# Optimization experiments

Hardware: AMD Instinct MI355X
Metric: run time of the kernel (lower is better)

## Reference

```python
import jax, jax.numpy as jnp
import numpy as np

DIM = 256; HEADS = 8; DEPTH = 2; DFF = 128
T = 64      # timesteps (transformer batch dim for s_transformer)
N = 2048    # total agents
S = 256     # number of segments (scenes)
L = 8       # agents per segment (N = S*L)
HD = DIM // HEADS
LN_EPS = 1e-5


def _ln(x, w, b):
    m = x.mean(-1, keepdims=True)
    v = x.var(-1, keepdims=True)
    return (x - m) / jnp.sqrt(v + LN_EPS) * w + b


def _mha(x, qkvw, qkvb, ow, ob):
    B, Sq, D = x.shape
    qkv = x @ qkvw.T + qkvb                      # [B,Sq,3D]
    q, k, v = jnp.split(qkv, 3, axis=-1)
    def sp(t):
        return t.reshape(B, Sq, HEADS, HD).transpose(0, 2, 1, 3)
    q, k, v = sp(q), sp(k), sp(v)
    a = jax.nn.softmax(jnp.einsum('bhqd,bhkd->bhqk', q, k) * (1.0 / (HD ** 0.5)))
    o = jnp.einsum('bhqk,bhkd->bhqd', a, v).transpose(0, 2, 1, 3).reshape(B, Sq, D)
    return o @ ow.T + ob


def _layer(x, qkvw, qkvb, ow, ob, l1w, l1b, l2w, l2b, ln1w, ln1b, ln2w, ln2b):
    # PyTorch TransformerEncoderLayer, post-norm, relu FFN
    x = _ln(x + _mha(x, qkvw, qkvb, ow, ob), ln1w, ln1b)
    h = jax.nn.relu(x @ l1w.T + l1b) @ l2w.T + l2b
    return _ln(x + h, ln2w, ln2b)


def _encoder(x, qkvw, qkvb, ow, ob, l1w, l1b, l2w, l2b, ln1w, ln1b, ln2w, ln2b):
    for i in range(DEPTH):
        x = _layer(x, qkvw[i], qkvb[i], ow[i], ob[i], l1w[i], l1b[i],
                   l2w[i], l2b[i], ln1w[i], ln1b[i], ln2w[i], ln2b[i])
    return x


def setup_inputs() -> dict:
    key = jax.random.key(0)
    ks = iter(jax.random.split(key, 64))
    def rn(shape, scale=0.05):
        return jax.random.normal(next(ks), shape, dtype=jnp.float32) * scale
    inp = {}
    inp['moveinfo'] = jax.random.normal(next(ks), (N, T, 2), dtype=jnp.float32)
    starts = jnp.arange(S, dtype=jnp.int32) * L
    inp['seq_start_end'] = jnp.stack([starts, starts + L], axis=1)  # [S,2]
    inp['w_in'] = rn((DIM, 2)); inp['b_in'] = rn((DIM,))
    for p in ('s', 't'):
        inp[p + '_qkvw'] = rn((DEPTH, 3 * DIM, DIM)); inp[p + '_qkvb'] = rn((DEPTH, 3 * DIM))
        inp[p + '_ow'] = rn((DEPTH, DIM, DIM)); inp[p + '_ob'] = rn((DEPTH, DIM))
        inp[p + '_l1w'] = rn((DEPTH, DFF, DIM)); inp[p + '_l1b'] = rn((DEPTH, DFF))
        inp[p + '_l2w'] = rn((DEPTH, DIM, DFF)); inp[p + '_l2b'] = rn((DEPTH, DIM))
        inp[p + '_ln1w'] = jnp.ones((DEPTH, DIM)); inp[p + '_ln1b'] = jnp.zeros((DEPTH, DIM))
        inp[p + '_ln2w'] = jnp.ones((DEPTH, DIM)); inp[p + '_ln2b'] = jnp.zeros((DEPTH, DIM))
    return inp


def reference(moveinfo, seq_start_end, w_in, b_in,
              s_qkvw, s_qkvb, s_ow, s_ob, s_l1w, s_l1b, s_l2w, s_l2b,
              s_ln1w, s_ln1b, s_ln2w, s_ln2b,
              t_qkvw, t_qkvb, t_ow, t_ob, t_l1w, t_l1b, t_l2w, t_l2b,
              t_ln1w, t_ln1b, t_ln2w, t_ln2b):
    # to_dim: Linear(2, dim) + exact GELU
    s_in = jax.nn.gelu(jnp.einsum('ntc,dc->ntd', moveinfo, w_in) + b_in, approximate=False)
    s_in = s_in.transpose(1, 0, 2)                       # [T, N, D]
    # gather equal-length segments: ragged loop batched as one attention call
    idx = seq_start_end[:, 0][:, None] + jnp.arange(L)   # [S, L]
    seg = s_in[:, idx, :].reshape(T * S, L, DIM)         # [T*S, L, D]
    cls = jnp.full((T * S, 1, DIM), 1e-5, dtype=s_in.dtype)
    x = jnp.concatenate([cls, seg], axis=1)              # [T*S, 1+L, D]
    x = _encoder(x, s_qkvw, s_qkvb, s_ow, s_ob, s_l1w, s_l1b, s_l2w, s_l2b,
                 s_ln1w, s_ln1b, s_ln2w, s_ln2b)
    t_in = x[:, 0, :].reshape(T, S, DIM).transpose(1, 0, 2)  # [S, T, D]
    out = _encoder(t_in, t_qkvw, t_qkvb, t_ow, t_ob, t_l1w, t_l1b, t_l2w, t_l2b,
                   t_ln1w, t_ln1b, t_ln2w, t_ln2b)
    return out
```

## Files before the change

### kernel.cpp

```cpp
#include <hip/hip_runtime.h>
#include <hip/hip_bf16.h>
#include <math.h>

typedef __bf16 bf16_t;
typedef float floatx4 __attribute__((ext_vector_type(4)));
typedef bf16_t bf16x8 __attribute__((ext_vector_type(8)));

typedef __attribute__((address_space(1))) void g_void;
typedef __attribute__((address_space(3))) void lds_void;

__device__ __forceinline__ void ldg_lds16(const bf16_t* g, bf16_t* l) {
    __builtin_amdgcn_global_load_lds((g_void*)g, (lds_void*)l, 16, 0, 0);
}

__device__ __forceinline__ void unpack4(uint2 r, float* o) {
    o[0] = __uint_as_float((r.x & 0xffffu) << 16); o[1] = __uint_as_float(r.x & 0xffff0000u);
    o[2] = __uint_as_float((r.y & 0xffffu) << 16); o[3] = __uint_as_float(r.y & 0xffff0000u);
}

__global__ void cvt_weights(const float* __restrict__ sqkvw, const float* __restrict__ sow,
                            const float* __restrict__ sl1w,  const float* __restrict__ sl2w,
                            const float* __restrict__ tqkvw, const float* __restrict__ tow,
                            const float* __restrict__ tl1w,  const float* __restrict__ tl2w,
                            bf16_t* __restrict__ dst) {
    int i = blockIdx.x * 256 + threadIdx.x;
    float v;
    if      (i <  393216) v = sqkvw[i];
    else if (i <  524288) v = sow  [i -  393216];
    else if (i <  589824) v = sl1w [i -  524288];
    else if (i <  655360) v = sl2w [i -  589824];
    else if (i < 1048576) v = tqkvw[i -  655360];
    else if (i < 1179648) v = tow  [i - 1048576];
    else if (i < 1245184) v = tl1w [i - 1179648];
    else                  v = tl2w [i - 1245184];
    dst[i] = (bf16_t)v;
}

__global__ void embed_k(const float* __restrict__ mv, const float* __restrict__ w_in,
                        const float* __restrict__ b_in, bf16_t* __restrict__ x, int b0) {
    int blk = blockIdx.x; int d = threadIdx.x;
    int tok = blk % 9; int lb = blk / 9;
    size_t oidx = (size_t)blk * 256 + d;
    if (tok == 0) { x[oidx] = (bf16_t)1e-5f; return; }
    int bb = b0 + lb; int t = bb >> 8; int s = bb & 255;
    int n = s * 8 + (tok - 1);
    float m0 = mv[((size_t)n * 64 + t) * 2];
    float m1 = mv[((size_t)n * 64 + t) * 2 + 1];
    float v = m0 * w_in[2 * d] + m1 * w_in[2 * d + 1] + b_in[d];
    v = 0.5f * v * (1.0f + erff(v * 0.70710678118654752f));
    x[oidx] = (bf16_t)v;
}

__global__ __launch_bounds__(256) void gemm_bt(const bf16_t* __restrict__ A,
                                               const bf16_t* __restrict__ W,
                                               const float* __restrict__ bias,
                                               bf16_t* __restrict__ C,
                                               int M, int N, int K, int relu) {
    __shared__ __align__(16) bf16_t As[8192];
    __shared__ __align__(16) bf16_t Ws[8192];
    int MT = M >> 7, NT = N >> 7;
    int g = blockIdx.x;
    int m_t, n_t;
    if ((MT & 7) == 0) {
        int x = g & 7, q = g >> 3;
        m_t = (q / NT) * 8 + x;
        n_t = q % NT;
    } else {
        m_t = g / NT; n_t = g % NT;
    }
    int tid = threadIdx.x;
    int lane = tid & 63;
    int wave = tid >> 6;
    int m0 = m_t * 128;
    int n0 = n_t * 128;
    int wm = (wave & 1) * 64;
    int wn = (wave >> 1) * 64;
    int arow = tid >> 2;
    int acol = (tid & 3) * 8;
    int fm = lane & 15;
    int fq = lane >> 4;

    floatx4 acc[4][4] = {};

    const bf16_t* Ag = A + (size_t)(m0 + arow) * K + acol;
    const bf16_t* Wg = W + (size_t)(n0 + arow) * K + acol;

    for (int k0 = 0; k0 < K; k0 += 64) {
        __syncthreads();
        ldg_lds16(Ag + k0,                       &As[tid * 8]);
        ldg_lds16(Ag + k0 + (size_t)64 * K,      &As[2048 + tid * 8]);
        ldg_lds16(Ag + k0 + 32,                  &As[4096 + tid * 8]);
        ldg_lds16(Ag + k0 + 32 + (size_t)64 * K, &As[6144 + tid * 8]);
        ldg_lds16(Wg + k0,                       &Ws[tid * 8]);
        ldg_lds16(Wg + k0 + (size_t)64 * K,      &Ws[2048 + tid * 8]);
        ldg_lds16(Wg + k0 + 32,                  &Ws[4096 + tid * 8]);
        ldg_lds16(Wg + k0 + 32 + (size_t)64 * K, &Ws[6144 + tid * 8]);
        __syncthreads();

#pragma unroll
        for (int sl = 0; sl < 2; sl++) {
            int base = sl * 4096;
            bf16x8 af[4], wf[4];
#pragma unroll
            for (int mi = 0; mi < 4; mi++)
                af[mi] = *(const bf16x8*)&As[base + (wm + mi * 16 + fm) * 32 + fq * 8];
#pragma unroll
            for (int ni = 0; ni < 4; ni++)
                wf[ni] = *(const bf16x8*)&Ws[base + (wn + ni * 16 + fm) * 32 + fq * 8];
#pragma unroll
            for (int mi = 0; mi < 4; mi++)
#pragma unroll
                for (int ni = 0; ni < 4; ni++)
                    acc[mi][ni] = __builtin_amdgcn_mfma_f32_16x16x32_bf16(wf[ni], af[mi], acc[mi][ni], 0, 0, 0);
        }
    }

#pragma unroll
    for (int mi = 0; mi < 4; mi++) {
        int row = m0 + wm + mi * 16 + fm;
#pragma unroll
        for (int ni = 0; ni < 4; ni++) {
            int colb = n0 + wn + ni * 16 + fq * 4;
            float4 b4 = *(const float4*)(bias + colb);
            float v0 = acc[mi][ni][0] + b4.x;
            float v1 = acc[mi][ni][1] + b4.y;
            float v2 = acc[mi][ni][2] + b4.z;
            float v3 = acc[mi][ni][3] + b4.w;
            if (relu) {
                v0 = fmaxf(v0, 0.f); v1 = fmaxf(v1, 0.f);
                v2 = fmaxf(v2, 0.f); v3 = fmaxf(v3, 0.f);
            }
            bf16_t t4[4] = {(bf16_t)v0, (bf16_t)v1, (bf16_t)v2, (bf16_t)v3};
            *(uint2*)(C + (size_t)row * N + colb) = *(uint2*)t4;
        }
    }
}

__device__ __forceinline__ void epi_resln64(
    floatx4 (&acc)[4][4], int m0, int wn, int fm, int fq, int wave,
    const float* __restrict__ bias, const bf16_t* __restrict__ res_bf,
    const float* __restrict__ res_f, const float* __restrict__ lnw,
    const float* __restrict__ lnb, bf16_t* out_bf, float* out_f,
    bf16_t* cls_bf, float* cls_f, int b0,
    float (*rs)[64], float (*rss)[64]) {
    float s[4] = {0.f, 0.f, 0.f, 0.f}, ss[4] = {0.f, 0.f, 0.f, 0.f};
#pragma unroll
    for (int mi = 0; mi < 4; mi++) {
        size_t row = (size_t)(m0 + mi * 16 + fm);
#pragma unroll
        for (int ni = 0; ni < 4; ni++) {
            int col = wn + ni * 16 + fq * 4;
            float4 b4 = *(const float4*)(bias + col);
            float r4[4];
            if (res_f) {
                float4 t = *(const float4*)(res_f + row * 256 + col);
                r4[0] = t.x; r4[1] = t.y; r4[2] = t.z; r4[3] = t.w;
            } else {
                unpack4(*(const uint2*)(res_bf + row * 256 + col), r4);
            }
            float v0 = acc[mi][ni][0] + b4.x + r4[0];
            float v1 = acc[mi][ni][1] + b4.y + r4[1];
            float v2 = acc[mi][ni][2] + b4.z + r4[2];
            float v3 = acc[mi][ni][3] + b4.w + r4[3];
            acc[mi][ni][0] = v0; acc[mi][ni][1] = v1;
            acc[mi][ni][2] = v2; acc[mi][ni][3] = v3;
            s[mi] += v0 + v1 + v2 + v3;
            ss[mi] += v0 * v0 + v1 * v1 + v2 * v2 + v3 * v3;
        }
    }
#pragma unroll
    for (int mi = 0; mi < 4; mi++) {
        s[mi]  += __shfl_xor(s[mi], 16);  s[mi]  += __shfl_xor(s[mi], 32);
        ss[mi] += __shfl_xor(ss[mi], 16); ss[mi] += __shfl_xor(ss[mi], 32);
    }
    if (fq == 0) {
#pragma unroll
        for (int mi = 0; mi < 4; mi++) {
            rs [wave][mi * 16 + fm] = s[mi];
            rss[wave][mi * 16 + fm] = ss[mi];
        }
    }
    __syncthreads();
#pragma unroll
    for (int mi = 0; mi < 4; mi++) {
        int lrow = mi * 16 + fm;
        int grow = m0 + lrow;
        size_t row = (size_t)grow;
        float mean = (rs[0][lrow] + rs[1][lrow] + rs[2][lrow] + rs[3][lrow]) * (1.f / 256.f);
        float var  = (rss[0][lrow] + rss[1][lrow] + rss[2][lrow] + rss[3][lrow]) * (1.f / 256.f)
                   - mean * mean;
        float inv = rsqrtf(var + 1e-5f);
        int is_cls = (cls_bf != nullptr) && (grow % 9 == 0);
        size_t di = 0;
        if (is_cls) {
            int bb = b0 + grow / 9;
            int tt = bb >> 8, sseg = bb & 255;
            di = ((size_t)(sseg * 64 + tt)) * 256;
        }
#pragma unroll
        for (int ni = 0; ni < 4; ni++) {
            int col = wn + ni * 16 + fq * 4;
            float4 w4 = *(const float4*)(lnw + col);
            float4 bl = *(const float4*)(lnb + col);
            float o0 = (acc[mi][ni][0] - mean) * inv * w4.x + bl.x;
            float o1 = (acc[mi][ni][1] - mean) * inv * w4.y + bl.y;
            float o2 = (acc[mi][ni][2] - mean) * inv * w4.z + bl.z;
            float o3 = (acc[mi][ni][3] - mean) * inv * w4.w + bl.w;
            if (out_bf) {
                bf16_t t4[4] = {(bf16_t)o0, (bf16_t)o1, (bf16_t)o2, (bf16_t)o3};
                *(uint2*)(out_bf + row * 256 + col) = *(uint2*)t4;
            }
            if (out_f) {
                float4 t; t.x = o0; t.y = o1; t.z = o2; t.w = o3;
                *(float4*)(out_f + row * 256 + col) = t;
            }
            if (is_cls) {
                bf16_t t4[4] = {(bf16_t)o0, (bf16_t)o1, (bf16_t)o2, (bf16_t)o3};
                *(uint2*)(cls_bf + di + col) = *(uint2*)t4;
                float4 t; t.x = o0; t.y = o1; t.z = o2; t.w = o3;
                *(float4*)(cls_f + di + col) = t;
            }
        }
    }
}

__global__ __launch_bounds__(256) void gemm_proj_ln(const bf16_t* __restrict__ A,
                                                    const bf16_t* __restrict__ W,
                                                    const float* __restrict__ bias,
                                                    const bf16_t* __restrict__ res_bf,
                                                    const float* __restrict__ res_f,
                                                    const float* __restrict__ lnw,
                                                    const float* __restrict__ lnb,
                                                    bf16_t* out_bf,
                                                    float* out_f) {
    __shared__ __align__(16) bf16_t As[4096];
    __shared__ __align__(16) bf16_t Ws[16384];
    __shared__ float rs[4][64], rss[4][64];
    int tid = threadIdx.x;
    int lane = tid & 63, wave = tid >> 6;
    int m0 = blockIdx.x * 64;
    int wn = wave * 64;
    int fm = lane & 15, fq = lane >> 4;
    floatx4 acc[4][4] = {};
    const bf16_t* Ag = A + (size_t)(m0 + (tid >> 2)) * 256 + (tid & 3) * 8;
    const bf16_t* Wg = W + (size_t)(tid >> 2) * 256 + (tid & 3) * 8;

    auto STAGE = [&](int r, int b) {
        int k = r * 32;
        ldg_lds16(Ag + k, &As[b * 2048 + tid * 8]);
#pragma unroll
        for (int j = 0; j < 4; j++)
            ldg_lds16(Wg + k + j * 16384, &Ws[b * 8192 + j * 2048 + tid * 8]);
    };
    auto COMPUTE = [&](int b) {
        bf16x8 af[4], wf[4];
#pragma unroll
        for (int mi = 0; mi < 4; mi++)
            af[mi] = *(const bf16x8*)&As[b * 2048 + (mi * 16 + fm) * 32 + fq * 8];
#pragma unroll
        for (int ni = 0; ni < 4; ni++)
            wf[ni] = *(const bf16x8*)&Ws[b * 8192 + (wn + ni * 16 + fm) * 32 + fq * 8];
#pragma unroll
        for (int mi = 0; mi < 4; mi++)
#pragma unroll
            for (int ni = 0; ni < 4; ni++)
                acc[mi][ni] = __builtin_amdgcn_mfma_f32_16x16x32_bf16(wf[ni], af[mi], acc[mi][ni], 0, 0, 0);
    };

    STAGE(0, 0);
    __syncthreads();
    for (int r = 0; r < 7; ++r) {
        STAGE(r + 1, (r + 1) & 1);
        COMPUTE(r & 1);
        __syncthreads();
    }
    COMPUTE(1);
    epi_resln64(acc, m0, wn, fm, fq, wave, bias, res_bf, res_f, lnw, lnb,
                out_bf, out_f, nullptr, nullptr, 0, rs, rss);
}

__global__ __launch_bounds__(256) void gemm_ffn_ln(const bf16_t* __restrict__ X,
                                                   const bf16_t* __restrict__ w1,
                                                   const float* __restrict__ b1,
                                                   const bf16_t* __restrict__ w2,
                                                   const float* __restrict__ b2,
                                                   const float* __restrict__ lnw,
                                                   const float* __restrict__ lnb,
                                                   const float* __restrict__ res_f,
                                                   bf16_t* out_bf, float* out_f,
                                                   bf16_t* cls_bf, float* cls_f, int b0) {
    __shared__ __align__(16) bf16_t As[4096];
    __shared__ __align__(16) bf16_t Ws[8192];
    __shared__ __align__(16) bf16_t Hs[10240];
    __shared__ float rs[4][64], rss[4][64];
    int tid = threadIdx.x, lane = tid & 63, wave = tid >> 6;
    int m0 = blockIdx.x * 64;
    int wn1 = wave * 32;
    int wn2 = wave * 64;
    int fm = lane & 15, fq = lane >> 4;
    floatx4 acc[4][2] = {};
    const bf16_t* Ag = X + (size_t)(m0 + (tid >> 2)) * 256 + (tid & 3) * 8;
    const bf16_t* Wg = w1 + (size_t)(tid >> 2) * 256 + (tid & 3) * 8;

    auto STAGE = [&](int r, int b) {
        int k = r * 32;
        ldg_lds16(Ag + k, &As[b * 2048 + tid * 8]);
#pragma unroll
        for (int j = 0; j < 2; j++)
            ldg_lds16(Wg + k + j * 16384, &Ws[b * 4096 + j * 2048 + tid * 8]);
    };
    auto COMPUTE = [&](int b) {
        bf16x8 af[4], wf[2];
#pragma unroll
        for (int mi = 0; mi < 4; mi++)
            af[mi] = *(const bf16x8*)&As[b * 2048 + (mi * 16 + fm) * 32 + fq * 8];
#pragma unroll
        for (int ni = 0; ni < 2; ni++)
            wf[ni] = *(const bf16x8*)&Ws[b * 4096 + (wn1 + ni * 16 + fm) * 32 + fq * 8];
#pragma unroll
        for (int mi = 0; mi < 4; mi++)
#pragma unroll
            for (int ni = 0; ni < 2; ni++)
                acc[mi][ni] = __builtin_amdgcn_mfma_f32_16x16x32_bf16(wf[ni], af[mi], acc[mi][ni], 0, 0, 0);
    };

    STAGE(0, 0);
    __syncthreads();
    for (int r = 0; r < 7; ++r) {
        STAGE(r + 1, (r + 1) & 1);
        COMPUTE(r & 1);
        __syncthreads();
    }
    COMPUTE(1);

#pragma unroll
    for (int mi = 0; mi < 4; mi++) {
        int row = mi * 16 + fm;
#pragma unroll
        for (int ni = 0; ni < 2; ni++) {
            int c = wn1 + ni * 16 + fq * 4;
            float4 b4 = *(const float4*)(b1 + c);
            bf16_t t4[4];
            t4[0] = (bf16_t)fmaxf(acc[mi][ni][0] + b4.x, 0.f);
            t4[1] = (bf16_t)fmaxf(acc[mi][ni][1] + b4.y, 0.f);
            t4[2] = (bf16_t)fmaxf(acc[mi][ni][2] + b4.z, 0.f);
            t4[3] = (bf16_t)fmaxf(acc[mi][ni][3] + b4.w, 0.f);
            *(uint2*)&Hs[(c >> 5) * 2560 + row * 40 + (c & 31)] = *(uint2*)t4;
        }
    }
    __syncthreads();
    floatx4 acc2[4][4] = {};
#pragma unroll
    for (int ks = 0; ks < 4; ks++) {
        bf16x8 af2[4];
#pragma unroll
        for (int mi = 0; mi < 4; mi++)
            af2[mi] = *(const bf16x8*)&Hs[ks * 2560 + (mi * 16 + fm) * 40 + fq * 8];
#pragma unroll
        for (int ni = 0; ni < 4; ni++) {
            bf16x8 wf2 = *(const bf16x8*)(w2 + (size_t)(wn2 + ni * 16 + fm) * 128 + ks * 32 + fq * 8);
#pragma unroll
            for (int mi = 0; mi < 4; mi++)
                acc2[mi][ni] = __builtin_amdgcn_mfma_f32_16x16x32_bf16(wf2, af2[mi], acc2[mi][ni], 0, 0, 0);
        }
    }
    epi_resln64(acc2, m0, wn2, fm, fq, wave, b2, X, res_f, lnw, lnb,
                out_bf, out_f, cls_bf, cls_f, b0, rs, rss);
}

__global__ __launch_bounds__(320) void attn9_k(const bf16_t* __restrict__ qkv,
                                               bf16_t* __restrict__ ao) {
    __shared__ __align__(16) bf16_t kv[36 * 512];
    int b = blockIdx.x; int tid = threadIdx.x;
    const bf16_t* src = qkv + (size_t)b * 27648;
    for (int c = tid; c < 2304; c += 320) {
        int row = c >> 6; int off = (c & 63) << 3;
        *(uint4*)&kv[row * 512 + off] = *(const uint4*)&src[row * 768 + 256 + off];
    }
    __syncthreads();
    if (tid < 288) {
        int s = tid / 72; int rem = tid - s * 72; int h = rem / 9; int i = rem - h * 9;
        const bf16_t* qp = src + (size_t)(s * 9 + i) * 768 + h * 32;
        float qf[32];
#pragma unroll
        for (int c = 0; c < 4; c++) {
            bf16x8 t8 = *(const bf16x8*)(qp + c * 8);
#pragma unroll
            for (int e = 0; e < 8; e++) qf[c * 8 + e] = (float)t8[e];
        }
        float sc[9]; float mx = -1e30f;
#pragma unroll
        for (int j = 0; j < 9; j++) {
            const bf16_t* kp = &kv[(s * 9 + j) * 512 + h * 32];
            float d = 0.f;
#pragma unroll
            for (int c = 0; c < 4; c++) {
                bf16x8 t8 = *(const bf16x8*)(kp + c * 8);
#pragma unroll
                for (int e = 0; e < 8; e++) d += qf[c * 8 + e] * (float)t8[e];
            }
            d *= 0.17677669529663687f;
            sc[j] = d; mx = fmaxf(mx, d);
        }
        float den = 0.f;
#pragma unroll
        for (int j = 0; j < 9; j++) { sc[j] = __expf(sc[j] - mx); den += sc[j]; }
        float inv = 1.0f / den;
        float of[32] = {};
#pragma unroll
        for (int j = 0; j < 9; j++) {
            const bf16_t* vp = &kv[(s * 9 + j) * 512 + 256 + h * 32];
            float w = sc[j];
#pragma unroll
            for (int c = 0; c < 4; c++) {
                bf16x8 t8 = *(const bf16x8*)(vp + c * 8);
#pragma unroll
                for (int e = 0; e < 8; e++) of[c * 8 + e] += w * (float)t8[e];
            }
        }
        bf16_t* dst = ao + ((size_t)(b * 4 + s) * 9 + i) * 256 + h * 32;
#pragma unroll
        for (int c = 0; c < 4; c++) {
            bf16x8 o8;
#pragma unroll
            for (int e = 0; e < 8; e++) o8[e] = (bf16_t)(of[c * 8 + e] * inv);
            *(bf16x8*)(dst + c * 8) = o8;
        }
    }
}

__global__ __launch_bounds__(256) void attn64_k(const bf16_t* __restrict__ qkv,
                                                bf16_t* __restrict__ ao) {
    __shared__ __align__(16) float kk[64 * 36];
    __shared__ __align__(16) float vv[64 * 36];
    __shared__ __align__(16) float pp[64 * 64];
    __shared__ float mloc[4 * 64];
    __shared__ float sloc[4 * 64];
    int s = blockIdx.x >> 3, h = blockIdx.x & 7;
    int t = threadIdx.x;
    int i = t & 63;
    int wq = t >> 6;

    {
        int r = t >> 2, c = t & 3;
        const bf16_t* kb = qkv + ((size_t)(s * 64 + r)) * 768 + h * 32 + 256 + c * 8;
        bf16x8 k8 = *(const bf16x8*)kb;
        bf16x8 v8 = *(const bf16x8*)(kb + 256);
        float* kd = &kk[r * 36 + c * 8];
        float* vd = &vv[r * 36 + c * 8];
#pragma unroll
        for (int e = 0; e < 8; e++) { kd[e] = (float)k8[e]; vd[e] = (float)v8[e]; }
    }
    const bf16_t* qb = qkv + ((size_t)(s * 64 + i)) * 768 + h * 32;
    float qf[32];
#pragma unroll
    for (int c = 0; c < 4; c++) {
        bf16x8 t8 = *(const bf16x8*)(qb + c * 8);
#pragma unroll
        for (int e = 0; e < 8; e++) qf[c * 8 + e] = (float)t8[e];
    }
    __syncthreads();

    float sc[16]; float mx = -1e30f;
#pragma unroll
    for (int jj = 0; jj < 16; jj++) {
        int j = wq * 16 + jj;
        const float* kr = &kk[j * 36];
        float d = 0.f;
#pragma unroll
        for (int c = 0; c < 8; c++) {
            float4 k4 = *(const float4*)(kr + c * 4);
            d += qf[c*4+0]*k4.x + qf[c*4+1]*k4.y + qf[c*4+2]*k4.z + qf[c*4+3]*k4.w;
        }
        d *= 0.17677669529663687f;
        sc[jj] = d; mx = fmaxf(mx, d);
    }
    float se = 0.f;
#pragma unroll
    for (int jj = 0; jj < 16; jj++) se += __expf(sc[jj] - mx);
    mloc[wq * 64 + i] = mx;
    sloc[wq * 64 + i] = se;
    __syncthreads();

    float m0 = mloc[i], m1 = mloc[64 + i], m2 = mloc[128 + i], m3 = mloc[192 + i];
    float gm = fmaxf(fmaxf(m0, m1), fmaxf(m2, m3));
    float D = sloc[i] * __expf(m0 - gm) + sloc[64 + i] * __expf(m1 - gm)
            + sloc[128 + i] * __expf(m2 - gm) + sloc[192 + i] * __expf(m3 - gm);

#pragma unroll
    for (int jj = 0; jj < 16; jj++)
        pp[(wq * 16 + jj) * 64 + i] = __expf(sc[jj] - gm);
    __syncthreads();

    float of[8] = {};
    for (int j = 0; j < 64; j++) {
        float w = pp[j * 64 + i];
        const float* vr = &vv[j * 36 + wq * 8];
        float4 va = *(const float4*)vr;
        float4 vb = *(const float4*)(vr + 4);
        of[0] += w * va.x; of[1] += w * va.y; of[2] += w * va.z; of[3] += w * va.w;
        of[4] += w * vb.x; of[5] += w * vb.y; of[6] += w * vb.z; of[7] += w * vb.w;
    }
    float invD = 1.0f / D;
    bf16_t o8[8];
#pragma unroll
    for (int e = 0; e < 8; e++) o8[e] = (bf16_t)(of[e] * invD);
    *(uint4*)(ao + ((size_t)(s * 64 + i)) * 256 + h * 32 + wq * 8) = *(uint4*)o8;
}

extern "C" void kernel_launch(void* const* d_in, const int* in_sizes, int n_in,
                              void* d_out, int out_size, void* d_ws, size_t ws_size,
                              hipStream_t stream) {
    const float* mv   = (const float*)d_in[0];
    const float* w_in = (const float*)d_in[2];
    const float* b_in = (const float*)d_in[3];
    const float* sp[12]; const float* tp[12];
    for (int i = 0; i < 12; i++) { sp[i] = (const float*)d_in[4 + i]; tp[i] = (const float*)d_in[16 + i]; }

    bf16_t* wbf = (bf16_t*)d_ws;
    bf16_t* txb = wbf + 1310720;
    float*  txf = (float*)(txb + 4194304);
    bf16_t* pool = (bf16_t*)(txf + 4194304);

    long long headB = 2621440LL + 8388608LL + 16777216LL;
    long long cand[5] = {16384, 8192, 4096, 2048, 1024};
    int BC = 1024;
    for (int c = 0; c < 5; c++) {
        long long poolB = cand[c] * 11520LL * 2;
        if (poolB < 33554432LL) poolB = 33554432LL;
        if ((size_t)(headB + poolB) <= ws_size) { BC = (int)cand[c]; break; }
    }

    cvt_weights<<<5120, 256, 0, stream>>>(sp[0], sp[2], sp[4], sp[6], tp[0], tp[2], tp[4], tp[6], wbf);

    const int M = BC * 9;
    const int MT64 = M / 64;
    bf16_t* xc    = pool;
    bf16_t* qkvb_ = pool + (long long)BC * 2304;
    bf16_t* aob   = qkvb_ + (long long)BC * 6912;

    for (int b0 = 0; b0 < 16384; b0 += BC) {
        embed_k<<<dim3(M), 256, 0, stream>>>(mv, w_in, b_in, xc, b0);
        for (int l = 0; l < 2; l++) {
            const bf16_t* wq = wbf + 0      + l * 196608;
            const bf16_t* wo = wbf + 393216 + l * 65536;
            const bf16_t* w1 = wbf + 524288 + l * 32768;
            const bf16_t* w2 = wbf + 589824 + l * 32768;
            gemm_bt<<<dim3((M / 128) * 6), 256, 0, stream>>>(xc, wq, sp[1] + l * 768, qkvb_, M, 768, 256, 0);
            attn9_k<<<dim3(BC / 4), 320, 0, stream>>>(qkvb_, aob);
            gemm_proj_ln<<<dim3(MT64), 256, 0, stream>>>(aob, wo, sp[3] + l * 256,
                                                         xc, (const float*)nullptr,
                                                         sp[8] + l * 256, sp[9] + l * 256,
                                                         xc, (float*)nullptr);
            if (l == 0)
                gemm_ffn_ln<<<dim3(MT64), 256, 0, stream>>>(xc, w1, sp[5] + l * 128,
                                                            w2, sp[7] + l * 256,
                                                            sp[10] + l * 256, sp[11] + l * 256,
                                                            (const float*)nullptr,
                                                            xc, (float*)nullptr,
                                                            (bf16_t*)nullptr, (float*)nullptr, 0);
            else
                gemm_ffn_ln<<<dim3(MT64), 256, 0, stream>>>(xc, w1, sp[5] + l * 128,
                                                            w2, sp[7] + l * 256,
                                                            sp[10] + l * 256, sp[11] + l * 256,
                                                            (const float*)nullptr,
                                                            (bf16_t*)nullptr, (float*)nullptr,
                                                            txb, txf, b0);
        }
    }

    bf16_t* tqkv = pool;
    bf16_t* tao  = pool + 12582912;
    for (int l = 0; l < 2; l++) {
        gemm_bt<<<dim3(128 * 6), 256, 0, stream>>>(txb, wbf + 655360 + l * 196608, tp[1] + l * 768,
                                                   tqkv, 16384, 768, 256, 0);
        attn64_k<<<dim3(2048), 256, 0, stream>>>(tqkv, tao);
        gemm_proj_ln<<<dim3(256), 256, 0, stream>>>(tao, wbf + 1048576 + l * 65536, tp[3] + l * 256,
                                                    (const bf16_t*)nullptr, txf,
                                                    tp[8] + l * 256, tp[9] + l * 256,
                                                    txb, txf);
        gemm_ffn_ln<<<dim3(256), 256, 0, stream>>>(txb, wbf + 1179648 + l * 32768, tp[5] + l * 128,
                                                   wbf + 1245184 + l * 32768, tp[7] + l * 256,
                                                   tp[10] + l * 256, tp[11] + l * 256,
                                                   txf,
                                                   (l == 0) ? txb : (bf16_t*)nullptr,
                                                   (l == 0) ? txf : (float*)d_out,
                                                   (bf16_t*)nullptr, (float*)nullptr, 0);
    }
}
```

Baseline: 1.057 ms.

## Fuse spatial attention output projection, LN1, FFN and LN2 into one kernel

Adds a proj_ffn_ln kernel that performs the attention output projection with residual and LayerNorm, keeps the normalized tile in LDS, then runs both FFN GEMMs and the second LayerNorm, writing the CLS rows for the temporal encoder. This replaces two launches per spatial layer and removes the global write and re-read of the intermediate activation. The FFN weights are now read straight from global memory rather than staged, and the larger LDS footprint (about 84KB) may lower occupancy.

```diff
diff --git a/kernel.cpp b/kernel.cpp
--- a/kernel.cpp
+++ b/kernel.cpp
@@ -219,6 +219,246 @@
                 *(uint2*)(cls_bf + di + col) = *(uint2*)t4;
                 float4 t; t.x = o0; t.y = o1; t.z = o2; t.w = o3;
                 *(float4*)(cls_f + di + col) = t;
+            }
+        }
+    }
+}
+
+__global__ __launch_bounds__(256) void proj_ffn_ln(const bf16_t* __restrict__ A,
+                                                   const bf16_t* __restrict__ Wo,
+                                                   const float* __restrict__ ob,
+                                                   const bf16_t* __restrict__ res,
+                                                   const float* __restrict__ ln1w,
+                                                   const float* __restrict__ ln1b,
+                                                   const bf16_t* __restrict__ w1,
+                                                   const float* __restrict__ b1,
+                                                   const bf16_t* __restrict__ w2,
+                                                   const float* __restrict__ b2,
+                                                   const float* __restrict__ ln2w,
+                                                   const float* __restrict__ ln2b,
+                                                   bf16_t* out_bf,
+                                                   bf16_t* cls_bf, float* cls_f, int b0) {
+    __shared__ __align__(16) bf16_t As[4096];
+    __shared__ __align__(16) bf16_t Ws[16384];
+    __shared__ __align__(16) bf16_t Xs[64 * 264];
+    __shared__ float rs[4][64], rss[4][64];
+    int tid = threadIdx.x, lane = tid & 63, wave = tid >> 6;
+    int m0 = blockIdx.x * 64;
+    int wn = wave * 64;
+    int wn1 = wave * 32;
+    int fm = lane & 15, fq = lane >> 4;
+
+    floatx4 acc[4][4] = {};
+    {
+        const bf16_t* Ag = A + (size_t)(m0 + (tid >> 2)) * 256 + (tid & 3) * 8;
+        const bf16_t* Wg = Wo + (size_t)(tid >> 2) * 256 + (tid & 3) * 8;
+        auto STAGE = [&](int r, int b) {
+            int k = r * 32;
+            ldg_lds16(Ag + k, &As[b * 2048 + tid * 8]);
+#pragma unroll
+            for (int j = 0; j < 4; j++)
+                ldg_lds16(Wg + k + j * 16384, &Ws[b * 8192 + j * 2048 + tid * 8]);
+        };
+        auto COMPUTE = [&](int b) {
+            bf16x8 af[4], wf[4];
+#pragma unroll
+            for (int mi = 0; mi < 4; mi++)
+                af[mi] = *(const bf16x8*)&As[b * 2048 + (mi * 16 + fm) * 32 + fq * 8];
+#pragma unroll
+            for (int ni = 0; ni < 4; ni++)
+                wf[ni] = *(const bf16x8*)&Ws[b * 8192 + (wn + ni * 16 + fm) * 32 + fq * 8];
+#pragma unroll
+            for (int mi = 0; mi < 4; mi++)
+#pragma unroll
+                for (int ni = 0; ni < 4; ni++)
+                    acc[mi][ni] = __builtin_amdgcn_mfma_f32_16x16x32_bf16(wf[ni], af[mi], acc[mi][ni], 0, 0, 0);
+        };
+        STAGE(0, 0);
+        __syncthreads();
+        for (int r = 0; r < 7; ++r) {
+            STAGE(r + 1, (r + 1) & 1);
+            COMPUTE(r & 1);
+            __syncthreads();
+        }
+        COMPUTE(1);
+    }
+
+    {
+        float s[4] = {0.f, 0.f, 0.f, 0.f}, ss[4] = {0.f, 0.f, 0.f, 0.f};
+#pragma unroll
+        for (int mi = 0; mi < 4; mi++) {
+            size_t row = (size_t)(m0 + mi * 16 + fm);
+#pragma unroll
+            for (int ni = 0; ni < 4; ni++) {
+                int col = wn + ni * 16 + fq * 4;
+                float4 b4 = *(const float4*)(ob + col);
+                float r4[4];
+                unpack4(*(const uint2*)(res + row * 256 + col), r4);
+                float v0 = acc[mi][ni][0] + b4.x + r4[0];
+                float v1 = acc[mi][ni][1] + b4.y + r4[1];
+                float v2 = acc[mi][ni][2] + b4.z + r4[2];
+                float v3 = acc[mi][ni][3] + b4.w + r4[3];
+                acc[mi][ni][0] = v0; acc[mi][ni][1] = v1;
+                acc[mi][ni][2] = v2; acc[mi][ni][3] = v3;
+                s[mi] += v0 + v1 + v2 + v3;
+                ss[mi] += v0 * v0 + v1 * v1 + v2 * v2 + v3 * v3;
+            }
+        }
+#pragma unroll
+        for (int mi = 0; mi < 4; mi++) {
+            s[mi]  += __shfl_xor(s[mi], 16);  s[mi]  += __shfl_xor(s[mi], 32);
+            ss[mi] += __shfl_xor(ss[mi], 16); ss[mi] += __shfl_xor(ss[mi], 32);
+        }
+        if (fq == 0) {
+#pragma unroll
+            for (int mi = 0; mi < 4; mi++) {
+                rs [wave][mi * 16 + fm] = s[mi];
+                rss[wave][mi * 16 + fm] = ss[mi];
+            }
+        }
+        __syncthreads();
+#pragma unroll
+        for (int mi = 0; mi < 4; mi++) {
+            int lrow = mi * 16 + fm;
+            float mean = (rs[0][lrow] + rs[1][lrow] + rs[2][lrow] + rs[3][lrow]) * (1.f / 256.f);
+            float var  = (rss[0][lrow] + rss[1][lrow] + rss[2][lrow] + rss[3][lrow]) * (1.f / 256.f)
+                       - mean * mean;
+            float inv = rsqrtf(var + 1e-5f);
+#pragma unroll
+            for (int ni = 0; ni < 4; ni++) {
+                int col = wn + ni * 16 + fq * 4;
+                float4 w4 = *(const float4*)(ln1w + col);
+                float4 bl = *(const float4*)(ln1b + col);
+                bf16_t t4[4];
+                t4[0] = (bf16_t)((acc[mi][ni][0] - mean) * inv * w4.x + bl.x);
+                t4[1] = (bf16_t)((acc[mi][ni][1] - mean) * inv * w4.y + bl.y);
+                t4[2] = (bf16_t)((acc[mi][ni][2] - mean) * inv * w4.z + bl.z);
+                t4[3] = (bf16_t)((acc[mi][ni][3] - mean) * inv * w4.w + bl.w);
+                *(uint2*)&Xs[lrow * 264 + col] = *(uint2*)t4;
+            }
+        }
+    }
+    __syncthreads();
+
+    floatx4 acc1[4][2] = {};
+#pragma unroll
+    for (int ks = 0; ks < 8; ks++) {
+        bf16x8 af[4];
+#pragma unroll
+        for (int mi = 0; mi < 4; mi++)
+            af[mi] = *(const bf16x8*)&Xs[(mi * 16 + fm) * 264 + ks * 32 + fq * 8];
+#pragma unroll
+        for (int ni = 0; ni < 2; ni++) {
+            bf16x8 wf = *(const bf16x8*)(w1 + (size_t)(wn1 + ni * 16 + fm) * 256 + ks * 32 + fq * 8);
+#pragma unroll
+            for (int mi = 0; mi < 4; mi++)
+                acc1[mi][ni] = __builtin_amdgcn_mfma_f32_16x16x32_bf16(wf, af[mi], acc1[mi][ni], 0, 0, 0);
+        }
+    }
+    bf16_t* Hs = Ws;
+#pragma unroll
+    for (int mi = 0; mi < 4; mi++) {
+        int row = mi * 16 + fm;
+#pragma unroll
+        for (int ni = 0; ni < 2; ni++) {
+            int c = wn1 + ni * 16 + fq * 4;
+            float4 b4 = *(const float4*)(b1 + c);
+            bf16_t t4[4];
+            t4[0] = (bf16_t)fmaxf(acc1[mi][ni][0] + b4.x, 0.f);
+            t4[1] = (bf16_t)fmaxf(acc1[mi][ni][1] + b4.y, 0.f);
+            t4[2] = (bf16_t)fmaxf(acc1[mi][ni][2] + b4.z, 0.f);
+            t4[3] = (bf16_t)fmaxf(acc1[mi][ni][3] + b4.w, 0.f);
+            *(uint2*)&Hs[(c >> 5) * 2560 + row * 40 + (c & 31)] = *(uint2*)t4;
+        }
+    }
+    __syncthreads();
+
+    floatx4 acc2[4][4] = {};
+#pragma unroll
+    for (int ks = 0; ks < 4; ks++) {
+        bf16x8 af2[4];
+#pragma unroll
+        for (int mi = 0; mi < 4; mi++)
+            af2[mi] = *(const bf16x8*)&Hs[ks * 2560 + (mi * 16 + fm) * 40 + fq * 8];
+#pragma unroll
+        for (int ni = 0; ni < 4; ni++) {
+            bf16x8 wf2 = *(const bf16x8*)(w2 + (size_t)(wn + ni * 16 + fm) * 128 + ks * 32 + fq * 8);
+#pragma unroll
+            for (int mi = 0; mi < 4; mi++)
+                acc2[mi][ni] = __builtin_amdgcn_mfma_f32_16x16x32_bf16(wf2, af2[mi], acc2[mi][ni], 0, 0, 0);
+        }
+    }
+
+    {
+        float s[4] = {0.f, 0.f, 0.f, 0.f}, ss[4] = {0.f, 0.f, 0.f, 0.f};
+#pragma unroll
+        for (int mi = 0; mi < 4; mi++) {
+            int lrow = mi * 16 + fm;
+#pragma unroll
+            for (int ni = 0; ni < 4; ni++) {
+                int col = wn + ni * 16 + fq * 4;
+                float4 b4 = *(const float4*)(b2 + col);
+                float r4[4];
+                unpack4(*(const uint2*)&Xs[lrow * 264 + col], r4);
+                float v0 = acc2[mi][ni][0] + b4.x + r4[0];
+                float v1 = acc2[mi][ni][1] + b4.y + r4[1];
+                float v2 = acc2[mi][ni][2] + b4.z + r4[2];
+                float v3 = acc2[mi][ni][3] + b4.w + r4[3];
+                acc2[mi][ni][0] = v0; acc2[mi][ni][1] = v1;
+                acc2[mi][ni][2] = v2; acc2[mi][ni][3] = v3;
+                s[mi] += v0 + v1 + v2 + v3;
+                ss[mi] += v0 * v0 + v1 * v1 + v2 * v2 + v3 * v3;
+            }
+        }
+#pragma unroll
+        for (int mi = 0; mi < 4; mi++) {
+            s[mi]  += __shfl_xor(s[mi], 16);  s[mi]  += __shfl_xor(s[mi], 32);
+            ss[mi] += __shfl_xor(ss[mi], 16); ss[mi] += __shfl_xor(ss[mi], 32);
+        }
+        __syncthreads();
+        if (fq == 0) {
+#pragma unroll
+            for (int mi = 0; mi < 4; mi++) {
+                rs [wave][mi * 16 + fm] = s[mi];
+                rss[wave][mi * 16 + fm] = ss[mi];
+            }
+        }
+        __syncthreads();
+#pragma unroll
+        for (int mi = 0; mi < 4; mi++) {
+            int lrow = mi * 16 + fm;
+            int grow = m0 + lrow;
+            size_t row = (size_t)grow;
+            float mean = (rs[0][lrow] + rs[1][lrow] + rs[2][lrow] + rs[3][lrow]) * (1.f / 256.f);
+            float var  = (rss[0][lrow] + rss[1][lrow] + rss[2][lrow] + rss[3][lrow]) * (1.f / 256.f)
+                       - mean * mean;
+            float inv = rsqrtf(var + 1e-5f);
+            int is_cls = (cls_bf != nullptr) && (grow % 9 == 0);
+            size_t di = 0;
+            if (is_cls) {
+                int bb = b0 + grow / 9;
+                int tt = bb >> 8, sseg = bb & 255;
+                di = ((size_t)(sseg * 64 + tt)) * 256;
+            }
+#pragma unroll
+            for (int ni = 0; ni < 4; ni++) {
+                int col = wn + ni * 16 + fq * 4;
+                float4 w4 = *(const float4*)(ln2w + col);
+                float4 bl = *(const float4*)(ln2b + col);
+                float o0 = (acc2[mi][ni][0] - mean) * inv * w4.x + bl.x;
+                float o1 = (acc2[mi][ni][1] - mean) * inv * w4.y + bl.y;
+                float o2 = (acc2[mi][ni][2] - mean) * inv * w4.z + bl.z;
+                float o3 = (acc2[mi][ni][3] - mean) * inv * w4.w + bl.w;
+                if (out_bf) {
+                    bf16_t t4[4] = {(bf16_t)o0, (bf16_t)o1, (bf16_t)o2, (bf16_t)o3};
+                    *(uint2*)(out_bf + row * 256 + col) = *(uint2*)t4;
+                }
+                if (is_cls) {
+                    bf16_t t4[4] = {(bf16_t)o0, (bf16_t)o1, (bf16_t)o2, (bf16_t)o3};
+                    *(uint2*)(cls_bf + di + col) = *(uint2*)t4;
+                    float4 t; t.x = o0; t.y = o1; t.z = o2; t.w = o3;
+                    *(float4*)(cls_f + di + col) = t;
+                }
             }
         }
     }
@@ -548,24 +788,14 @@
             const bf16_t* w2 = wbf + 589824 + l * 32768;
             gemm_bt<<<dim3((M / 128) * 6), 256, 0, stream>>>(xc, wq, sp[1] + l * 768, qkvb_, M, 768, 256, 0);
             attn9_k<<<dim3(BC / 4), 320, 0, stream>>>(qkvb_, aob);
-            gemm_proj_ln<<<dim3(MT64), 256, 0, stream>>>(aob, wo, sp[3] + l * 256,
-                                                         xc, (const float*)nullptr,
-                                                         sp[8] + l * 256, sp[9] + l * 256,
-                                                         xc, (float*)nullptr);
-            if (l == 0)
-                gemm_ffn_ln<<<dim3(MT64), 256, 0, stream>>>(xc, w1, sp[5] + l * 128,
-                                                            w2, sp[7] + l * 256,
-                                                            sp[10] + l * 256, sp[11] + l * 256,
-                                                            (const float*)nullptr,
-                                                            xc, (float*)nullptr,
-                                                            (bf16_t*)nullptr, (float*)nullptr, 0);
-            else
-                gemm_ffn_ln<<<dim3(MT64), 256, 0, stream>>>(xc, w1, sp[5] + l * 128,
-                                                            w2, sp[7] + l * 256,
-                                                            sp[10] + l * 256, sp[11] + l * 256,
-                                                            (const float*)nullptr,
-                                                            (bf16_t*)nullptr, (float*)nullptr,
-                                                            txb, txf, b0);
+            proj_ffn_ln<<<dim3(MT64), 256, 0, stream>>>(aob, wo, sp[3] + l * 256,
+                                                        xc, sp[8] + l * 256, sp[9] + l * 256,
+                                                        w1, sp[5] + l * 128,
+                                                        w2, sp[7] + l * 256,
+                                                        sp[10] + l * 256, sp[11] + l * 256,
+                                                        (l == 0) ? xc : (bf16_t*)nullptr,
+                                                        (l == 0) ? (bf16_t*)nullptr : txb,
+                                                        (l == 0) ? (float*)nullptr : txf, b0);
         }
     }
 
```

After: 969.4 us (median of 2 runs). -8.3%, faster.
